# Kernel optimization log

Measured on AMD Instinct MI355X. Metric: run time of the kernel, lower is better.

Reference implementation:

```python
import jax, jax.numpy as jnp
import numpy as np

B, N, M, D = 8, 4096, 4096, 2


def setup_inputs() -> dict:
    key = jax.random.key(0)
    k1, k2 = jax.random.split(key)
    x = jax.random.normal(k1, (B, N, D), dtype=jnp.float32)
    target = jax.random.normal(k2, (B, M, D), dtype=jnp.float32)
    return {"x": x, "target": target}


def reference(x, target):
    # Pairwise squared Euclidean distances [B, N, M] via the expansion
    # ||a-b||^2 = ||a||^2 + ||b||^2 - 2 a.b  (matmul-friendly form).
    x2 = jnp.sum(x * x, axis=-1)            # [B, N]
    t2 = jnp.sum(target * target, axis=-1)  # [B, M]
    cross = jnp.einsum("bnd,bmd->bnm", x, target)  # [B, N, M]
    d2 = x2[:, :, None] + t2[:, None, :] - 2.0 * cross
    d2 = jnp.maximum(d2, 0.0)  # numerical floor before sqrt
    # tree1.query(array2[i]): for each target point, distance to nearest x point.
    d_t_to_x = jnp.sqrt(jnp.min(d2, axis=1))  # [B, M]
    # tree2.query(array1[i]): for each x point, distance to nearest target point.
    d_x_to_t = jnp.sqrt(jnp.min(d2, axis=2))  # [B, N]
    # sum over batch of (mean1 + mean2)/B == mean of per-batch means (equal sizes).
    return jnp.mean(d_t_to_x) + jnp.mean(d_x_to_t)
```

## Files before the change

### kernel.cpp

```cpp
#include <hip/hip_runtime.h>
#include <math.h>

#define NPTS  4096
#define BQ    64
#define RQ    16
#define SLOTS 4
#define NS    128
#define CHUNK 32
#define CF4   16
#define PCF4  17

__global__ __launch_bounds__(512, 6) void chamfer_main(
    const float* __restrict__ x, const float* __restrict__ tgt,
    float* __restrict__ partials)
{
    __shared__ float4 sm[NS * PCF4];
    __shared__ float  red[8 * BQ];

    const int bx  = blockIdx.x;
    const int dir = bx >> 9;
    const int b   = (bx >> 6) & 7;
    const int qt  = bx & 63;
    const int t   = threadIdx.x;
    const int lane = t & 63, w = t >> 6;

    const float* qarr = dir ? tgt : x;
    const float* sarr = dir ? x   : tgt;

    const float4* sp4 = (const float4*)(sarr + b * (NPTS * 2));
    #pragma unroll
    for (int k = 0; k < 4; ++k) {
        const int i = t + k * 512;
        sm[i + (i >> 4)] = sp4[i];
    }

    const int slot = t & (SLOTS - 1);
    const int s    = t >> 2;
    const float2* qp = (const float2*)(qarr + b * (NPTS * 2));
    float nx[RQ], ny[RQ], m[RQ];
    #pragma unroll
    for (int r = 0; r < RQ; ++r) {
        const float2 p = qp[qt * BQ + slot + SLOTS * r];
        nx[r] = -2.f * p.x;
        ny[r] = -2.f * p.y;
        m[r]  = INFINITY;
    }
    __syncthreads();

    const float4* tp = sm + s * PCF4;
    #pragma unroll 4
    for (int j = 0; j < CF4; ++j) {
        const float4 t4 = tp[j];
        const float z0 = fmaf(t4.x, t4.x, t4.y * t4.y);
        const float z1 = fmaf(t4.z, t4.z, t4.w * t4.w);
        #pragma unroll
        for (int r = 0; r < RQ; ++r) {
            const float d0 = fmaf(nx[r], t4.x, fmaf(ny[r], t4.y, z0));
            const float d1 = fmaf(nx[r], t4.z, fmaf(ny[r], t4.w, z1));
            m[r] = fminf(fminf(m[r], d0), d1);
        }
    }

    #pragma unroll
    for (int r = 0; r < RQ; ++r)
        m[r] += 0.25f * fmaf(nx[r], nx[r], ny[r] * ny[r]);

    #pragma unroll
    for (int r = 0; r < RQ; ++r) {
        m[r] = fminf(m[r], __shfl_xor(m[r], 4));
        m[r] = fminf(m[r], __shfl_xor(m[r], 8));
        m[r] = fminf(m[r], __shfl_xor(m[r], 16));
        m[r] = fminf(m[r], __shfl_xor(m[r], 32));
    }
    if (lane < SLOTS) {
        #pragma unroll
        for (int r = 0; r < RQ; ++r) red[w * BQ + lane + SLOTS * r] = m[r];
    }
    __syncthreads();

    if (t < BQ) {
        float mm = red[t];
        #pragma unroll
        for (int ww = 1; ww < 8; ++ww) mm = fminf(mm, red[ww * BQ + t]);
        float v = sqrtf(fmaxf(mm, 0.f));
        v += __shfl_down(v, 32);
        v += __shfl_down(v, 16);
        v += __shfl_down(v, 8);
        v += __shfl_down(v, 4);
        v += __shfl_down(v, 2);
        v += __shfl_down(v, 1);
        if (t == 0) partials[bx] = v;
    }
}

__global__ __launch_bounds__(256) void chamfer_final(
    const float* __restrict__ partials, float* __restrict__ out)
{
    __shared__ float red[256];
    const int tid = threadIdx.x;
    float v = partials[tid] + partials[tid + 256] +
              partials[tid + 512] + partials[tid + 768];
    red[tid] = v;
    __syncthreads();
    if (tid < 64) {
        float s = red[tid] + red[tid + 64] + red[tid + 128] + red[tid + 192];
        s += __shfl_down(s, 32);
        s += __shfl_down(s, 16);
        s += __shfl_down(s, 8);
        s += __shfl_down(s, 4);
        s += __shfl_down(s, 2);
        s += __shfl_down(s, 1);
        if (tid == 0) out[0] = s * (1.0f / 32768.0f);
    }
}

extern "C" void kernel_launch(void* const* d_in, const int* in_sizes, int n_in,
                              void* d_out, int out_size, void* d_ws, size_t ws_size,
                              hipStream_t stream) {
    const float* x   = (const float*)d_in[0];
    const float* tgt = (const float*)d_in[1];
    float* partials  = (float*)d_ws;
    float* out       = (float*)d_out;

    chamfer_main<<<dim3(1024), dim3(512), 0, stream>>>(x, tgt, partials);
    chamfer_final<<<dim3(1),   dim3(256), 0, stream>>>(partials, out);
}
```

Baseline: 26.24 us.

## Use packed FMA and min3 in chamfer inner loop with retiled query slots

After: 28.04 us. 1.07x slower.

```diff
diff --git a/kernel.cpp b/kernel.cpp
--- a/kernel.cpp
+++ b/kernel.cpp
@@ -3,18 +3,30 @@
 
 #define NPTS  4096
 #define BQ    64
-#define RQ    16
-#define SLOTS 4
-#define NS    128
-#define CHUNK 32
-#define CF4   16
-#define PCF4  17
+#define RQ    8
+#define SLOTS 8
+#define NS    64
+#define NPAIR 32
+#define PSTR  33
+
+typedef float f32x2 __attribute__((ext_vector_type(2)));
+
+static __device__ __forceinline__ f32x2 pk_fma2(f32x2 a, f32x2 b, f32x2 c) {
+    f32x2 d;
+    asm("v_pk_fma_f32 %0, %1, %2, %3" : "=v"(d) : "v"(a), "v"(b), "v"(c));
+    return d;
+}
+static __device__ __forceinline__ float min3f(float a, float b, float c) {
+    float d;
+    asm("v_min3_f32 %0, %1, %2, %3" : "=v"(d) : "v"(a), "v"(b), "v"(c));
+    return d;
+}
 
 __global__ __launch_bounds__(512, 6) void chamfer_main(
     const float* __restrict__ x, const float* __restrict__ tgt,
     float* __restrict__ partials)
 {
-    __shared__ float4 sm[NS * PCF4];
+    __shared__ float4 sm[NS * PSTR];
     __shared__ float  red[8 * BQ];
 
     const int bx  = blockIdx.x;
@@ -31,43 +43,47 @@
     #pragma unroll
     for (int k = 0; k < 4; ++k) {
         const int i = t + k * 512;
-        sm[i + (i >> 4)] = sp4[i];
+        sm[i + (i >> 5)] = sp4[i];
     }
 
     const int slot = t & (SLOTS - 1);
-    const int s    = t >> 2;
+    const int s    = t >> 3;
     const float2* qp = (const float2*)(qarr + b * (NPTS * 2));
-    float nx[RQ], ny[RQ], m[RQ];
+    f32x2 qx2[RQ], qy2[RQ];
+    float m[RQ];
     #pragma unroll
     for (int r = 0; r < RQ; ++r) {
         const float2 p = qp[qt * BQ + slot + SLOTS * r];
-        nx[r] = -2.f * p.x;
-        ny[r] = -2.f * p.y;
-        m[r]  = INFINITY;
+        const float nx = -2.f * p.x, ny = -2.f * p.y;
+        qx2[r].x = nx; qx2[r].y = nx;
+        qy2[r].x = ny; qy2[r].y = ny;
+        m[r] = INFINITY;
     }
     __syncthreads();
 
-    const float4* tp = sm + s * PCF4;
-    #pragma unroll 4
-    for (int j = 0; j < CF4; ++j) {
+    const float4* tp = sm + s * PSTR;
+    #pragma unroll 2
+    for (int j = 0; j < NPAIR; ++j) {
         const float4 t4 = tp[j];
-        const float z0 = fmaf(t4.x, t4.x, t4.y * t4.y);
-        const float z1 = fmaf(t4.z, t4.z, t4.w * t4.w);
+        f32x2 XX; XX.x = t4.x; XX.y = t4.z;
+        f32x2 YY; YY.x = t4.y; YY.y = t4.w;
+        f32x2 Z;
+        Z.x = fmaf(t4.x, t4.x, t4.y * t4.y);
+        Z.y = fmaf(t4.z, t4.z, t4.w * t4.w);
         #pragma unroll
         for (int r = 0; r < RQ; ++r) {
-            const float d0 = fmaf(nx[r], t4.x, fmaf(ny[r], t4.y, z0));
-            const float d1 = fmaf(nx[r], t4.z, fmaf(ny[r], t4.w, z1));
-            m[r] = fminf(fminf(m[r], d0), d1);
+            f32x2 d = pk_fma2(YY, qy2[r], Z);
+            d = pk_fma2(XX, qx2[r], d);
+            m[r] = min3f(m[r], d.x, d.y);
         }
     }
 
     #pragma unroll
     for (int r = 0; r < RQ; ++r)
-        m[r] += 0.25f * fmaf(nx[r], nx[r], ny[r] * ny[r]);
+        m[r] += 0.25f * fmaf(qx2[r].x, qx2[r].x, qy2[r].x * qy2[r].x);
 
     #pragma unroll
     for (int r = 0; r < RQ; ++r) {
-        m[r] = fminf(m[r], __shfl_xor(m[r], 4));
         m[r] = fminf(m[r], __shfl_xor(m[r], 8));
         m[r] = fminf(m[r], __shfl_xor(m[r], 16));
         m[r] = fminf(m[r], __shfl_xor(m[r], 32));
@@ -98,9 +114,8 @@
 {
     __shared__ float red[256];
     const int tid = threadIdx.x;
-    float v = partials[tid] + partials[tid + 256] +
-              partials[tid + 512] + partials[tid + 768];
-    red[tid] = v;
+    red[tid] = partials[tid] + partials[tid + 256] +
+               partials[tid + 512] + partials[tid + 768];
     __syncthreads();
     if (tid < 64) {
         float s = red[tid] + red[tid + 64] + red[tid + 128] + red[tid + 192];
```
